# Kernel optimization log

Hardware: AMD Instinct MI355X
Metric: run time of the kernel (lower is better)

Reference implementation:

```python
import jax, jax.numpy as jnp
import numpy as np

N_BINS = 11
Q_LEN = 20
EPS = 1e-8


def setup_inputs() -> dict:
    key = jax.random.key(0)
    ks = jax.random.split(key, 5)
    L, B, S, H = 13, 16, 512, 768
    hidden_size = 5
    n_all_layers = L + 1  # forward duplicates hidden_states[0]
    comb_in = H + hidden_size * n_all_layers  # 838
    return {
        "hidden_states": jax.random.normal(ks[0], (L, B, S, H), dtype=jnp.float32),
        "W_hist": jax.random.normal(ks[1], (hidden_size, N_BINS), dtype=jnp.float32) * 0.1,
        "b_hist": jax.random.normal(ks[2], (hidden_size,), dtype=jnp.float32) * 0.1,
        "W_comb": jax.random.normal(ks[3], (1, comb_in), dtype=jnp.float32) * 0.05,
        "b_comb": jax.random.normal(ks[4], (1,), dtype=jnp.float32) * 0.05,
    }


def _cosine_simmat(layers):
    # layers: [L, B, S, H] -> sim: [L, B, 20, S-20]
    q = layers[:, :, :Q_LEN, :]
    d = layers[:, :, Q_LEN:, :]
    dots = jnp.einsum("lbqh,lbdh->lbqd", q, d)
    qn = jnp.linalg.norm(q, axis=-1)  # [L,B,20]
    dn = jnp.linalg.norm(d, axis=-1)  # [L,B,D]
    denom = jnp.maximum(qn[:, :, :, None] * dn[:, :, None, :], EPS)
    return dots / denom


def _histogram(sim):
    # sim: [L, B, Q, D] -> hist: [L, B, n_bins], normalized counts
    bounds = jnp.linspace(-1.0, 1.0, N_BINS + 1)
    lo, hi = bounds[:-1], bounds[1:]
    inbin = (sim[..., None] >= lo) & (sim[..., None] < hi)  # [L,B,Q,D,n_bins]
    counts = jnp.sum(inbin.astype(sim.dtype), axis=(2, 3))  # [L,B,n_bins]
    return counts / (sim.shape[2] * sim.shape[3])


def reference(hidden_states, W_hist, b_hist, W_comb, b_comb):
    # hidden_states: [13, B, S, H]; all_layers = [layer0] + all 13 -> 14 layers
    all_layers = jnp.concatenate([hidden_states[:1], hidden_states], axis=0)  # [14,B,S,H]
    cls_output = hidden_states[-1][:, 0, :]  # [B, H]

    sim = _cosine_simmat(all_layers)         # [14,B,20,S-20]
    hist = _histogram(sim)                   # [14,B,11]
    hfeat = jnp.einsum("lbn,on->lbo", hist, W_hist) + b_hist  # [14,B,5]

    B = hidden_states.shape[1]
    histogram_features = jnp.transpose(hfeat, (1, 0, 2)).reshape(B, -1)  # [B, 14*5]
    combined = jnp.concatenate([cls_output, histogram_features], axis=-1)  # [B, 838]
    return combined @ W_comb.T + b_comb  # [B, 1]
```

## Files before the change

### kernel.cpp

```cpp
#include <hip/hip_runtime.h>
#include <math.h>

#define HH    768
#define QL    20
#define SS    512
#define DD    492
#define NBATCH 16
#define NLAYER 13
#define NBINS 11
#define DSPLIT 4
#define BROWS 123
#define BN    128
#define BK    64
#define QPAD  776
#define BPAD  72

typedef __attribute__((ext_vector_type(8))) short bf16x8;
typedef __attribute__((ext_vector_type(4))) float f32x4;

__device__ inline unsigned int pk2bf(float a, float b) {
    unsigned int ua = __float_as_uint(a);
    unsigned int ub = __float_as_uint(b);
    ua = (ua + 0x7fffu + ((ua >> 16) & 1u)) >> 16;
    ub = (ub + 0x7fffu + ((ub >> 16) & 1u)) >> 16;
    return ua | (ub << 16);
}

__global__ __launch_bounds__(256, 2)
void gemm_hist_kernel(const float* __restrict__ hs, float* __restrict__ counts) {
    const int l = blockIdx.x, b = blockIdx.y, dc = blockIdx.z;
    const float* __restrict__ base = hs + (size_t)(l * NBATCH + b) * SS * HH;
    const int t = threadIdx.x;
    const int wave = t >> 6, lane = t & 63;
    const int quad = lane >> 4, m16 = lane & 15;

    __shared__ unsigned short sQ[32 * QPAD];
    __shared__ unsigned short sB[BN * BPAD];
    __shared__ float s_qn2[QL], s_qn[QL];
    __shared__ float s_dn2[BN], s_dn[BN];
    __shared__ int   s_hist[NBINS];

    if (t < QL) s_qn2[t] = 0.f;
    if (t < BN) s_dn2[t] = 0.f;
    if (t < NBINS) s_hist[t] = 0;
    for (int i = t; i < 12 * QPAD; i += 256) sQ[20 * QPAD + i] = 0;
    __syncthreads();

    #pragma unroll
    for (int j = 0; j < 15; ++j) {
        int i = t + 256 * j;
        int r = i / 192, c4 = i - r * 192;
        float4 v = *reinterpret_cast<const float4*>(base + r * HH + c4 * 4);
        atomicAdd(&s_qn2[r], v.x * v.x + v.y * v.y + v.z * v.z + v.w * v.w);
        uint2 hw;
        hw.x = pk2bf(v.x, v.y);
        hw.y = pk2bf(v.z, v.w);
        *reinterpret_cast<uint2*>(&sQ[r * QPAD + c4 * 4]) = hw;
    }

    f32x4 acc[2][2] = {{{0,0,0,0},{0,0,0,0}},{{0,0,0,0},{0,0,0,0}}};
    float dnacc[8];
    #pragma unroll
    for (int j = 0; j < 8; ++j) dnacc[j] = 0.f;

    const int rowbase = t >> 4;
    const int kf = t & 15;

    for (int kt = 0; kt < HH / BK; ++kt) {
        const int kbase = kt * BK;
        __syncthreads();
        #pragma unroll
        for (int j = 0; j < 8; ++j) {
            int row = rowbase + 16 * j;
            int grow = QL + dc * BROWS + (row < BROWS ? row : BROWS - 1);
            float4 v = *reinterpret_cast<const float4*>(base + (size_t)grow * HH + kbase + kf * 4);
            dnacc[j] += v.x * v.x + v.y * v.y + v.z * v.z + v.w * v.w;
            uint2 hw;
            hw.x = pk2bf(v.x, v.y);
            hw.y = pk2bf(v.z, v.w);
            *reinterpret_cast<uint2*>(&sB[row * BPAD + kf * 4]) = hw;
        }
        __syncthreads();
        #pragma unroll
        for (int ks = 0; ks < BK; ks += 32) {
            const int ka = kbase + ks + quad * 8;
            const int kb = ks + quad * 8;
            bf16x8 a0 = *reinterpret_cast<const bf16x8*>(&sQ[m16 * QPAD + ka]);
            bf16x8 a1 = *reinterpret_cast<const bf16x8*>(&sQ[(16 + m16) * QPAD + ka]);
            bf16x8 b0 = *reinterpret_cast<const bf16x8*>(&sB[(wave * 32 + m16) * BPAD + kb]);
            bf16x8 b1 = *reinterpret_cast<const bf16x8*>(&sB[(wave * 32 + 16 + m16) * BPAD + kb]);
            acc[0][0] = __builtin_amdgcn_mfma_f32_16x16x32_bf16(a0, b0, acc[0][0], 0, 0, 0);
            acc[0][1] = __builtin_amdgcn_mfma_f32_16x16x32_bf16(a0, b1, acc[0][1], 0, 0, 0);
            acc[1][0] = __builtin_amdgcn_mfma_f32_16x16x32_bf16(a1, b0, acc[1][0], 0, 0, 0);
            acc[1][1] = __builtin_amdgcn_mfma_f32_16x16x32_bf16(a1, b1, acc[1][1], 0, 0, 0);
        }
    }

    #pragma unroll
    for (int j = 0; j < 8; ++j) atomicAdd(&s_dn2[rowbase + 16 * j], dnacc[j]);
    __syncthreads();
    if (t < QL) s_qn[t] = sqrtf(s_qn2[t]);
    if (t < BN) s_dn[t] = sqrtf(s_dn2[t]);
    __syncthreads();

    int cnt[NBINS];
    #pragma unroll
    for (int k = 0; k < NBINS; ++k) cnt[k] = 0;
    #pragma unroll
    for (int mt = 0; mt < 2; ++mt) {
        #pragma unroll
        for (int nt = 0; nt < 2; ++nt) {
            int d = wave * 32 + nt * 16 + m16;
            #pragma unroll
            for (int r = 0; r < 4; ++r) {
                int q = mt * 16 + quad * 4 + r;
                if (q < QL && d < BROWS) {
                    float sim = acc[mt][nt][r] / fmaxf(s_qn[q] * s_dn[d], 1e-8f);
                    int bin = (int)floorf((sim + 1.0f) * 5.5f);
                    #pragma unroll
                    for (int k = 0; k < NBINS; ++k) cnt[k] += (bin == k) ? 1 : 0;
                }
            }
        }
    }
    #pragma unroll
    for (int k = 0; k < NBINS; ++k) {
        int v = cnt[k];
        for (int off = 32; off > 0; off >>= 1) v += __shfl_down(v, off, 64);
        if (lane == 0 && v != 0) atomicAdd(&s_hist[k], v);
    }
    __syncthreads();
    if (t < NBINS)
        counts[(((size_t)(l * NBATCH + b)) * DSPLIT + dc) * NBINS + t] = (float)s_hist[t];
}

__global__ __launch_bounds__(256)
void finalize_kernel(const float* __restrict__ hs,
                     const float* __restrict__ Wh,
                     const float* __restrict__ bh,
                     const float* __restrict__ Wc,
                     const float* __restrict__ bc,
                     const float* __restrict__ counts,
                     float* __restrict__ out) {
    const int b = blockIdx.x;
    const int t = threadIdx.x;
    float p = 0.f;

    const float* cls = hs + ((size_t)(12 * NBATCH + b)) * SS * HH;
    for (int j = t; j < HH; j += 256) p += cls[j] * Wc[j];

    if (t < 14 * NBINS) {
        const int l  = t / NBINS;
        const int n  = t % NBINS;
        const int lp = (l == 0) ? 0 : l - 1;
        float hsum = 0.f;
        #pragma unroll
        for (int dcc = 0; dcc < DSPLIT; ++dcc)
            hsum += counts[(((size_t)lp * NBATCH + b) * DSPLIT + dcc) * NBINS + n];
        float hist = hsum * (1.0f / (float)(QL * DD));
        float coef = 0.f;
        #pragma unroll
        for (int o = 0; o < 5; ++o) coef += Wc[HH + l * 5 + o] * Wh[o * NBINS + n];
        p += hist * coef;
    }

    if (t == 0) {
        float s = bc[0];
        for (int l = 0; l < 14; ++l)
            for (int o = 0; o < 5; ++o) s += Wc[HH + l * 5 + o] * bh[o];
        p += s;
    }

    __shared__ float red[256];
    red[t] = p;
    __syncthreads();
    for (int off = 128; off > 0; off >>= 1) {
        if (t < off) red[t] += red[t + off];
        __syncthreads();
    }
    if (t == 0) out[b] = red[0];
}

extern "C" void kernel_launch(void* const* d_in, const int* in_sizes, int n_in,
                              void* d_out, int out_size, void* d_ws, size_t ws_size,
                              hipStream_t stream) {
    const float* hs = (const float*)d_in[0];
    const float* Wh = (const float*)d_in[1];
    const float* bh = (const float*)d_in[2];
    const float* Wc = (const float*)d_in[3];
    const float* bc = (const float*)d_in[4];
    float* counts = (float*)d_ws;
    float* out    = (float*)d_out;

    dim3 g1(NLAYER, NBATCH, DSPLIT);
    gemm_hist_kernel<<<g1, 256, 0, stream>>>(hs, counts);
    finalize_kernel<<<NBATCH, 256, 0, stream>>>(hs, Wh, bh, Wc, bc, counts, out);
}
```

Baseline: 480.0 us.

## Stream Q tiles per K-step with double-buffered register-prefetch pipeline

Q rows are no longer staged in full up front; they are loaded per K-tile alongside the D rows into double-buffered shared memory. Next-tile global loads are issued into registers before the MFMA work on the current tile, then converted and stored afterwards, leaving one barrier per iteration. Shrinking sQ cuts LDS use, and launch bounds rise to 3 blocks per CU for more occupancy. The cost is more register pressure from the prefetch buffers, which could cause spills under the tighter bound.

```diff
diff --git a/kernel.cpp b/kernel.cpp
--- a/kernel.cpp
+++ b/kernel.cpp
@@ -12,7 +12,7 @@
 #define BROWS 123
 #define BN    128
 #define BK    64
-#define QPAD  776
+#define NKT   (HH / BK)
 #define BPAD  72
 
 typedef __attribute__((ext_vector_type(8))) short bf16x8;
@@ -26,7 +26,7 @@
     return ua | (ub << 16);
 }
 
-__global__ __launch_bounds__(256, 2)
+__global__ __launch_bounds__(256, 3)
 void gemm_hist_kernel(const float* __restrict__ hs, float* __restrict__ counts) {
     const int l = blockIdx.x, b = blockIdx.y, dc = blockIdx.z;
     const float* __restrict__ base = hs + (size_t)(l * NBATCH + b) * SS * HH;
@@ -34,8 +34,8 @@
     const int wave = t >> 6, lane = t & 63;
     const int quad = lane >> 4, m16 = lane & 15;
 
-    __shared__ unsigned short sQ[32 * QPAD];
-    __shared__ unsigned short sB[BN * BPAD];
+    __shared__ unsigned short sQ[2][32][BPAD];
+    __shared__ unsigned short sB[2][BN][BPAD];
     __shared__ float s_qn2[QL], s_qn[QL];
     __shared__ float s_dn2[BN], s_dn[BN];
     __shared__ int   s_hist[NBINS];
@@ -43,61 +43,114 @@
     if (t < QL) s_qn2[t] = 0.f;
     if (t < BN) s_dn2[t] = 0.f;
     if (t < NBINS) s_hist[t] = 0;
-    for (int i = t; i < 12 * QPAD; i += 256) sQ[20 * QPAD + i] = 0;
-    __syncthreads();
-
-    #pragma unroll
-    for (int j = 0; j < 15; ++j) {
-        int i = t + 256 * j;
-        int r = i / 192, c4 = i - r * 192;
-        float4 v = *reinterpret_cast<const float4*>(base + r * HH + c4 * 4);
-        atomicAdd(&s_qn2[r], v.x * v.x + v.y * v.y + v.z * v.z + v.w * v.w);
+    for (int i = t; i < 2 * 12 * BPAD; i += 256) {
+        int bufi = i / (12 * BPAD);
+        int rem  = i - bufi * (12 * BPAD);
+        sQ[bufi][20 + rem / BPAD][rem % BPAD] = 0;
+    }
+
+    const int  kf  = t & 15;
+    const int  qr0 = t >> 4;
+    const bool q1  = (t < 64);
+    const int  qr1 = 16 + (t >> 4);
+    const int  rb  = t >> 4;
+    int  growB[8];
+    bool bvld[8];
+    #pragma unroll
+    for (int j = 0; j < 8; ++j) {
+        int row  = rb + 16 * j;
+        bvld[j]  = (row < BROWS);
+        growB[j] = QL + dc * BROWS + (row < BROWS ? row : BROWS - 1);
+    }
+
+    float qn0 = 0.f, qn1 = 0.f;
+    float dnacc[8];
+    #pragma unroll
+    for (int j = 0; j < 8; ++j) dnacc[j] = 0.f;
+    f32x4 acc[2][2] = {{{0,0,0,0},{0,0,0,0}},{{0,0,0,0},{0,0,0,0}}};
+
+    {
+        float4 pq0, pq1, pb[8];
+        pq0 = *reinterpret_cast<const float4*>(base + qr0 * HH + kf * 4);
+        if (q1) pq1 = *reinterpret_cast<const float4*>(base + qr1 * HH + kf * 4);
+        #pragma unroll
+        for (int j = 0; j < 8; ++j) {
+            float4 z = {0.f, 0.f, 0.f, 0.f};
+            pb[j] = bvld[j] ? *reinterpret_cast<const float4*>(base + (size_t)growB[j] * HH + kf * 4) : z;
+        }
+        qn0 += pq0.x*pq0.x + pq0.y*pq0.y + pq0.z*pq0.z + pq0.w*pq0.w;
         uint2 hw;
-        hw.x = pk2bf(v.x, v.y);
-        hw.y = pk2bf(v.z, v.w);
-        *reinterpret_cast<uint2*>(&sQ[r * QPAD + c4 * 4]) = hw;
-    }
-
-    f32x4 acc[2][2] = {{{0,0,0,0},{0,0,0,0}},{{0,0,0,0},{0,0,0,0}}};
-    float dnacc[8];
-    #pragma unroll
-    for (int j = 0; j < 8; ++j) dnacc[j] = 0.f;
-
-    const int rowbase = t >> 4;
-    const int kf = t & 15;
-
-    for (int kt = 0; kt < HH / BK; ++kt) {
-        const int kbase = kt * BK;
-        __syncthreads();
+        hw.x = pk2bf(pq0.x, pq0.y); hw.y = pk2bf(pq0.z, pq0.w);
+        *reinterpret_cast<uint2*>(&sQ[0][qr0][kf * 4]) = hw;
+        if (q1) {
+            qn1 += pq1.x*pq1.x + pq1.y*pq1.y + pq1.z*pq1.z + pq1.w*pq1.w;
+            hw.x = pk2bf(pq1.x, pq1.y); hw.y = pk2bf(pq1.z, pq1.w);
+            *reinterpret_cast<uint2*>(&sQ[0][qr1][kf * 4]) = hw;
+        }
         #pragma unroll
         for (int j = 0; j < 8; ++j) {
-            int row = rowbase + 16 * j;
-            int grow = QL + dc * BROWS + (row < BROWS ? row : BROWS - 1);
-            float4 v = *reinterpret_cast<const float4*>(base + (size_t)grow * HH + kbase + kf * 4);
-            dnacc[j] += v.x * v.x + v.y * v.y + v.z * v.z + v.w * v.w;
-            uint2 hw;
-            hw.x = pk2bf(v.x, v.y);
-            hw.y = pk2bf(v.z, v.w);
-            *reinterpret_cast<uint2*>(&sB[row * BPAD + kf * 4]) = hw;
-        }
-        __syncthreads();
+            dnacc[j] += pb[j].x*pb[j].x + pb[j].y*pb[j].y + pb[j].z*pb[j].z + pb[j].w*pb[j].w;
+            uint2 w2;
+            w2.x = pk2bf(pb[j].x, pb[j].y); w2.y = pk2bf(pb[j].z, pb[j].w);
+            *reinterpret_cast<uint2*>(&sB[0][rb + 16 * j][kf * 4]) = w2;
+        }
+    }
+    __syncthreads();
+
+    int cur = 0;
+    for (int kt = 0; kt < NKT; ++kt) {
+        float4 nq0, nq1, nb[8];
+        const bool pf = (kt + 1 < NKT);
+        if (pf) {
+            const int kb = (kt + 1) * BK;
+            nq0 = *reinterpret_cast<const float4*>(base + qr0 * HH + kb + kf * 4);
+            if (q1) nq1 = *reinterpret_cast<const float4*>(base + qr1 * HH + kb + kf * 4);
+            #pragma unroll
+            for (int j = 0; j < 8; ++j) {
+                float4 z = {0.f, 0.f, 0.f, 0.f};
+                nb[j] = bvld[j] ? *reinterpret_cast<const float4*>(base + (size_t)growB[j] * HH + kb + kf * 4) : z;
+            }
+        }
         #pragma unroll
         for (int ks = 0; ks < BK; ks += 32) {
-            const int ka = kbase + ks + quad * 8;
-            const int kb = ks + quad * 8;
-            bf16x8 a0 = *reinterpret_cast<const bf16x8*>(&sQ[m16 * QPAD + ka]);
-            bf16x8 a1 = *reinterpret_cast<const bf16x8*>(&sQ[(16 + m16) * QPAD + ka]);
-            bf16x8 b0 = *reinterpret_cast<const bf16x8*>(&sB[(wave * 32 + m16) * BPAD + kb]);
-            bf16x8 b1 = *reinterpret_cast<const bf16x8*>(&sB[(wave * 32 + 16 + m16) * BPAD + kb]);
+            const int ko = ks + quad * 8;
+            bf16x8 a0 = *reinterpret_cast<const bf16x8*>(&sQ[cur][m16][ko]);
+            bf16x8 a1 = *reinterpret_cast<const bf16x8*>(&sQ[cur][16 + m16][ko]);
+            bf16x8 b0 = *reinterpret_cast<const bf16x8*>(&sB[cur][wave * 32 + m16][ko]);
+            bf16x8 b1 = *reinterpret_cast<const bf16x8*>(&sB[cur][wave * 32 + 16 + m16][ko]);
             acc[0][0] = __builtin_amdgcn_mfma_f32_16x16x32_bf16(a0, b0, acc[0][0], 0, 0, 0);
             acc[0][1] = __builtin_amdgcn_mfma_f32_16x16x32_bf16(a0, b1, acc[0][1], 0, 0, 0);
             acc[1][0] = __builtin_amdgcn_mfma_f32_16x16x32_bf16(a1, b0, acc[1][0], 0, 0, 0);
             acc[1][1] = __builtin_amdgcn_mfma_f32_16x16x32_bf16(a1, b1, acc[1][1], 0, 0, 0);
         }
-    }
-
-    #pragma unroll
-    for (int j = 0; j < 8; ++j) atomicAdd(&s_dn2[rowbase + 16 * j], dnacc[j]);
+        if (pf) {
+            const int nxt = cur ^ 1;
+            qn0 += nq0.x*nq0.x + nq0.y*nq0.y + nq0.z*nq0.z + nq0.w*nq0.w;
+            uint2 hw;
+            hw.x = pk2bf(nq0.x, nq0.y); hw.y = pk2bf(nq0.z, nq0.w);
+            *reinterpret_cast<uint2*>(&sQ[nxt][qr0][kf * 4]) = hw;
+            if (q1) {
+                qn1 += nq1.x*nq1.x + nq1.y*nq1.y + nq1.z*nq1.z + nq1.w*nq1.w;
+                hw.x = pk2bf(nq1.x, nq1.y); hw.y = pk2bf(nq1.z, nq1.w);
+                *reinterpret_cast<uint2*>(&sQ[nxt][qr1][kf * 4]) = hw;
+            }
+            #pragma unroll
+            for (int j = 0; j < 8; ++j) {
+                dnacc[j] += nb[j].x*nb[j].x + nb[j].y*nb[j].y + nb[j].z*nb[j].z + nb[j].w*nb[j].w;
+                uint2 w2;
+                w2.x = pk2bf(nb[j].x, nb[j].y); w2.y = pk2bf(nb[j].z, nb[j].w);
+                *reinterpret_cast<uint2*>(&sB[nxt][rb + 16 * j][kf * 4]) = w2;
+            }
+        }
+        __syncthreads();
+        cur ^= 1;
+    }
+
+    atomicAdd(&s_qn2[qr0], qn0);
+    if (q1) atomicAdd(&s_qn2[qr1], qn1);
+    #pragma unroll
+    for (int j = 0; j < 8; ++j)
+        if (bvld[j]) atomicAdd(&s_dn2[rb + 16 * j], dnacc[j]);
     __syncthreads();
     if (t < QL) s_qn[t] = sqrtf(s_qn2[t]);
     if (t < BN) s_dn[t] = sqrtf(s_dn2[t]);
```

Measured after the change: 474.2 us. No clear change (-1.2%).
